# Kernel optimization log

Measured on AMD Instinct MI355X. Metric: run time of the kernel, lower is better.

## Reference

```python
import jax, jax.numpy as jnp
import numpy as np

EMBED_DIM = 1024
NUM_HEADS = 16
HEAD_DIM = EMBED_DIM // NUM_HEADS


def setup_inputs() -> dict:
    key = jax.random.key(0)
    ks = jax.random.split(key, 5)
    B, N, C = 2, 2048, EMBED_DIM
    s = 0.02
    return {
        "x": jax.random.normal(ks[0], (B, N, C), dtype=jnp.float32),
        "w_qkv": jax.random.normal(ks[1], (C, 3 * C), dtype=jnp.float32) * s,
        "b_qkv": jax.random.normal(ks[2], (3 * C,), dtype=jnp.float32) * s,
        "w_proj": jax.random.normal(ks[3], (C, C), dtype=jnp.float32) * s,
        "b_proj": jax.random.normal(ks[4], (C,), dtype=jnp.float32) * s,
    }


def reference(x, w_qkv, b_qkv, w_proj, b_proj):
    B, N, C = x.shape
    H, D = NUM_HEADS, C // NUM_HEADS
    scale = D ** -0.5
    qkv = x @ w_qkv + b_qkv                      # [B,N,3C]
    qkv = qkv.reshape(B, N, 3, H, D).transpose(2, 0, 3, 1, 4)  # [3,B,H,N,D]
    q, k, v = qkv[0] * scale, qkv[1], qkv[2]
    attn = jnp.einsum("bhnd,bhmd->bhnm", q, k)   # [B,H,N,N]
    attn = jax.nn.softmax(attn, axis=-1)
    out = jnp.einsum("bhnm,bhmd->bhnd", attn, v)  # [B,H,N,D]
    out = out.transpose(0, 2, 1, 3).reshape(B, N, C)
    return out @ w_proj + b_proj
```

## Files before the change

### kernel.cpp

```cpp
#include <hip/hip_runtime.h>

typedef short bf16x8 __attribute__((ext_vector_type(8)));
typedef float f32x4 __attribute__((ext_vector_type(4)));
typedef float f32x16 __attribute__((ext_vector_type(16)));
typedef unsigned short ushort8 __attribute__((ext_vector_type(8)));
typedef unsigned short ushort4v __attribute__((ext_vector_type(4)));
typedef unsigned int uint4v __attribute__((ext_vector_type(4)));
typedef unsigned short u16;

__device__ inline u16 f2bf(float f) {
  unsigned int u = __float_as_uint(f);
  u += 0x7fffu + ((u >> 16) & 1u);
  return (u16)(u >> 16);
}

__device__ inline unsigned cvt_pk_bf16(float lo, float hi2) {
  unsigned r;
  asm("v_cvt_pk_bf16_f32 %0, %1, %2" : "=v"(r) : "v"(lo), "v"(hi2));
  return r;
}

__device__ inline void perm32swap(unsigned& a, unsigned& b) {
  asm("v_permlane32_swap_b32 %0, %1" : "+v"(a), "+v"(b));
}

__device__ inline void gload_lds16(const u16* g, u16* l) {
  __builtin_amdgcn_global_load_lds(
      (const __attribute__((address_space(1))) unsigned int*)g,
      (__attribute__((address_space(3))) unsigned int*)l, 16, 0, 0);
}

__global__ __launch_bounds__(256) void cvt_bf16(const float* __restrict__ in,
                                                u16* __restrict__ out, int n) {
  int i = (blockIdx.x * 256 + threadIdx.x) * 8;
  if (i >= n) return;
  float4 a = *(const float4*)(in + i);
  float4 b = *(const float4*)(in + i + 4);
  ushort8 o;
  o[0] = f2bf(a.x); o[1] = f2bf(a.y); o[2] = f2bf(a.z); o[3] = f2bf(a.w);
  o[4] = f2bf(b.x); o[5] = f2bf(b.y); o[6] = f2bf(b.z); o[7] = f2bf(b.w);
  *(ushort8*)(out + i) = o;
}

__global__ __launch_bounds__(256) void trans_w(const float* __restrict__ W,
                                               u16* __restrict__ Wt, int K, int N) {
  const int k0 = blockIdx.x * 64, n0 = blockIdx.y * 64;
  const int tx = threadIdx.x & 63, ty = threadIdx.x >> 6;
  __shared__ float t[64][65];
#pragma unroll
  for (int i = 0; i < 16; ++i) {
    int r = i * 4 + ty;
    t[r][tx] = W[(size_t)(k0 + r) * N + n0 + tx];
  }
  __syncthreads();
#pragma unroll
  for (int i = 0; i < 16; ++i) {
    int r = i * 4 + ty;
    Wt[(size_t)(n0 + r) * K + k0 + tx] = f2bf(t[tx][r]);
  }
}

template <int MODE>
__global__ __launch_bounds__(256) void gemm_bt(
    const u16* __restrict__ A, const u16* __restrict__ Bt, int M, int N, int K,
    const float* __restrict__ bias, float* __restrict__ outF,
    u16* __restrict__ Qb, u16* __restrict__ Kb, u16* __restrict__ Vb) {
  const int bm = blockIdx.x * 128;
  const int bn = blockIdx.y * 128;
  const int tid = threadIdx.x;
  const int wid = tid >> 6;
  const int lr = tid & 15;
  const int lg = (tid >> 4) & 3;
  const int wr = wid >> 1, wc = wid & 1;

  __shared__ u16 smem[32768];
  u16* Ab0 = smem;
  u16* Ab1 = smem + 8192;
  u16* Bb0 = smem + 16384;
  u16* Bb1 = smem + 24576;

  f32x4 acc[4][4] = {};

  const int rowi = tid >> 3;
  const int sslot = ((tid & 7) ^ (rowi & 7)) * 8;
  const u16* Ag = A + (size_t)bm * K;
  const u16* Bg = Bt + (size_t)bn * K;
  const int nkt = K >> 6;

  auto stage = [&](u16* Ad, u16* Bd, int kt) {
    const int kof = kt << 6;
#pragma unroll
    for (int i = 0; i < 4; ++i) {
      const int row = i * 32 + rowi;
      gload_lds16(Ag + (size_t)row * K + kof + sslot, Ad + (i * 32 + wid * 8) * 64);
      gload_lds16(Bg + (size_t)row * K + kof + sslot, Bd + (i * 32 + wid * 8) * 64);
    }
  };

  stage(Ab0, Bb0, 0);
  __syncthreads();

  for (int kt = 0; kt < nkt; ++kt) {
    const int p = kt & 1;
    const char* Ard = (const char*)(p ? Ab1 : Ab0);
    const char* Brd = (const char*)(p ? Bb1 : Bb0);
    bf16x8 af[4], bfr[4];
#pragma unroll
    for (int t = 0; t < 4; ++t) {
      const int ra = wr * 64 + t * 16 + lr;
      const int rb = wc * 64 + t * 16 + lr;
      af[t] = *(const bf16x8*)(Ard + ra * 128 + ((lg * 16) ^ ((ra & 7) << 4)));
      bfr[t] = *(const bf16x8*)(Brd + rb * 128 + ((lg * 16) ^ ((rb & 7) << 4)));
    }
    if (kt + 1 < nkt) stage(p ? Ab0 : Ab1, p ? Bb0 : Bb1, kt + 1);
    __builtin_amdgcn_s_setprio(1);
#pragma unroll
    for (int mt = 0; mt < 4; ++mt)
#pragma unroll
      for (int nt = 0; nt < 4; ++nt)
        acc[mt][nt] = __builtin_amdgcn_mfma_f32_16x16x32_bf16(
            af[mt], bfr[nt], acc[mt][nt], 0, 0, 0);
    __builtin_amdgcn_s_setprio(0);
#pragma unroll
    for (int t = 0; t < 4; ++t) {
      const int ra = wr * 64 + t * 16 + lr;
      const int rb = wc * 64 + t * 16 + lr;
      af[t] = *(const bf16x8*)(Ard + ra * 128 + ((64 + lg * 16) ^ ((ra & 7) << 4)));
      bfr[t] = *(const bf16x8*)(Brd + rb * 128 + ((64 + lg * 16) ^ ((rb & 7) << 4)));
    }
    __builtin_amdgcn_s_setprio(1);
#pragma unroll
    for (int mt = 0; mt < 4; ++mt)
#pragma unroll
      for (int nt = 0; nt < 4; ++nt)
        acc[mt][nt] = __builtin_amdgcn_mfma_f32_16x16x32_bf16(
            af[mt], bfr[nt], acc[mt][nt], 0, 0, 0);
    __builtin_amdgcn_s_setprio(0);
    __syncthreads();
  }

  if (MODE == 1) {
#pragma unroll
    for (int mt = 0; mt < 4; ++mt) {
      const int row0 = bm + wr * 64 + mt * 16 + lg * 4;
#pragma unroll
      for (int nt = 0; nt < 4; ++nt) {
        const int col = bn + wc * 64 + nt * 16 + lr;
        const float bv = bias[col];
#pragma unroll
        for (int r = 0; r < 4; ++r)
          outF[(size_t)(row0 + r) * N + col] = acc[mt][nt][r] + bv;
      }
    }
    return;
  }

  u16* T = smem;
  const int which = bn >> 10;

  if (which == 2) {
#pragma unroll
    for (int nt = 0; nt < 4; ++nt) {
      const int cl = wc * 64 + nt * 16 + lr;
      const float bv = bias[bn + cl];
#pragma unroll
      for (int mt = 0; mt < 4; ++mt) {
        const int rlb = wr * 128 + mt * 32 + lg * 8;
        ushort4v pk;
#pragma unroll
        for (int r = 0; r < 4; ++r) pk[r] = f2bf(acc[mt][nt][r] + bv);
        *(ushort4v*)((char*)T + cl * 256 + (rlb ^ ((cl & 7) << 4))) = pk;
      }
    }
  } else {
    const float sc = (which == 0) ? 0.18033688f : 1.0f;
#pragma unroll
    for (int mt = 0; mt < 4; ++mt) {
      const int rl0 = wr * 64 + mt * 16 + lg * 4;
#pragma unroll
      for (int nt = 0; nt < 4; ++nt) {
        const int cl = wc * 64 + nt * 16 + lr;
        const float bv = bias[bn + cl];
#pragma unroll
        for (int r = 0; r < 4; ++r) {
          const int rl = rl0 + r;
          *(u16*)((char*)T + rl * 256 + ((cl * 2) ^ ((rl & 7) << 4))) =
              f2bf((acc[mt][nt][r] + bv) * sc);
        }
      }
    }
  }
  __syncthreads();

  const int b = bm >> 11;
  const int nbase = bm & 2047;
  if (which == 0) {
#pragma unroll
    for (int i = 0; i < 8; ++i) {
      const int c = i * 256 + tid;
      const int rl = c >> 4, dch = c & 15;
      uint4v v =
          *(const uint4v*)((const char*)T + rl * 256 + ((dch * 16) ^ ((rl & 7) << 4)));
      const int bh = b * 16 + (bn >> 6) + (dch >> 3);
      *(uint4v*)(Qb + ((size_t)bh * 2048 + nbase + rl) * 64 + (dch & 7) * 8) = v;
    }
  } else if (which == 1) {
#pragma unroll
    for (int i = 0; i < 8; ++i) {
      const int c = i * 256 + tid;
      const int lane = c & 63, s = (c >> 6) & 7, ktl = (c >> 9) & 1, hl = c >> 10;
      const int lq = lane & 31, hi2 = lane >> 5;
      const int rl = ktl * 64 + (s & 1) * 32 + lq;
      const int cc = hl * 128 + (s >> 1) * 32 + hi2 * 16;
      uint4v v = *(const uint4v*)((const char*)T + rl * 256 + (cc ^ ((rl & 7) << 4)));
      const int bh = b * 16 + ((bn & 1023) >> 6) + hl;
      const int kt2 = (nbase >> 6) + ktl;
      *(uint4v*)(Kb + ((((size_t)bh * 32 + kt2) * 8 + s) * 64 + lane) * 8) = v;
    }
  } else {
#pragma unroll
    for (int i = 0; i < 8; ++i) {
      const int c = i * 256 + tid;
      const int lane = c & 63, s = (c >> 6) & 7, ktl = (c >> 9) & 1, hl = c >> 10;
      const int lq = lane & 31, hi2 = lane >> 5;
      const int cl = hl * 64 + (s & 1) * 32 + lq;
      const int cc = ktl * 128 + (s >> 1) * 32 + hi2 * 16;
      uint4v v = *(const uint4v*)((const char*)T + cl * 256 + (cc ^ ((cl & 7) << 4)));
      const int bh = b * 16 + ((bn & 1023) >> 6) + hl;
      const int kt2 = (nbase >> 6) + ktl;
      *(uint4v*)(Vb + ((((size_t)bh * 32 + kt2) * 8 + s) * 64 + lane) * 8) = v;
    }
  }
}

__global__ __launch_bounds__(256, 2) void flash_attn10(const u16* __restrict__ Qb,
                                                       const u16* __restrict__ Kp,
                                                       const u16* __restrict__ Vp,
                                                       u16* __restrict__ AO) {
  const int bh = blockIdx.x & 31;
  const int qt = blockIdx.x >> 5;
  const int tid = threadIdx.x;
  const int w = tid >> 6;
  const int lane = tid & 63;
  const int lq = lane & 31;
  const int hi = lane >> 5;
  const int q0 = qt * 128 + w * 32;

  __shared__ u16 Kld[2][4096];
  __shared__ u16 Vld[2][4096];

  const u16* Qg = Qb + ((size_t)bh * 2048 + q0 + lq) * 64 + 8 * hi;
  bf16x8 qf[4];
#pragma unroll
  for (int t = 0; t < 4; ++t) qf[t] = *(const bf16x8*)(Qg + 16 * t);

  const u16* Kg = Kp + (size_t)bh * (32 * 4096);
  const u16* Vg = Vp + (size_t)bh * (32 * 4096);

  f32x16 ot0 = {}, ot1 = {};
  float lacc[8] = {};

  auto stage = [&](int p, int kt) {
    const size_t src = (size_t)kt * 4096;
    gload_lds16(Kg + src + tid * 8, &Kld[p][tid * 8]);
    gload_lds16(Kg + src + 2048 + tid * 8, &Kld[p][2048 + tid * 8]);
    gload_lds16(Vg + src + tid * 8, &Vld[p][tid * 8]);
    gload_lds16(Vg + src + 2048 + tid * 8, &Vld[p][2048 + tid * 8]);
  };

  stage(0, 0);
  __syncthreads();

  for (int kt = 0; kt < 32; ++kt) {
    const int p = kt & 1;
    if (kt < 31) stage(p ^ 1, kt + 1);

    bf16x8 kf[8];
#pragma unroll
    for (int s = 0; s < 8; ++s)
      kf[s] = *(const bf16x8*)&Kld[p][s * 512 + lane * 8];

    f32x16 sa = {}, sb = {};
    __builtin_amdgcn_s_setprio(1);
#pragma unroll
    for (int t = 0; t < 4; ++t) {
      sa = __builtin_amdgcn_mfma_f32_32x32x16_bf16(kf[2 * t], qf[t], sa, 0, 0, 0);
      sb = __builtin_amdgcn_mfma_f32_32x32x16_bf16(kf[2 * t + 1], qf[t], sb, 0, 0, 0);
    }
    __builtin_amdgcn_s_setprio(0);

    bf16x8 vf[8];
#pragma unroll
    for (int s = 0; s < 8; ++s)
      vf[s] = *(const bf16x8*)&Vld[p][s * 512 + lane * 8];

#pragma unroll
    for (int r = 0; r < 16; ++r) {
      sa[r] = __builtin_amdgcn_exp2f(sa[r]);
      sb[r] = __builtin_amdgcn_exp2f(sb[r]);
    }
#pragma unroll
    for (int r = 0; r < 8; ++r)
      lacc[r] += (sa[r] + sa[r + 8]) + (sb[r] + sb[r + 8]);

    unsigned Ua[8], Ub[8];
#pragma unroll
    for (int s = 0; s < 4; ++s)
#pragma unroll
      for (int m2 = 0; m2 < 2; ++m2) {
        Ua[s * 2 + m2] = cvt_pk_bf16(sa[4 * s + 2 * m2], sa[4 * s + 2 * m2 + 1]);
        Ub[s * 2 + m2] = cvt_pk_bf16(sb[4 * s + 2 * m2], sb[4 * s + 2 * m2 + 1]);
      }
    bf16x8 pfrag[4];
#pragma unroll
    for (int t = 0; t < 4; ++t) {
      const unsigned* U = (t < 2) ? Ua : Ub;
      const int tt = t & 1;
      unsigned w0 = U[(2 * tt) * 2 + 0], w2 = U[(2 * tt + 1) * 2 + 0];
      unsigned w1 = U[(2 * tt) * 2 + 1], w3 = U[(2 * tt + 1) * 2 + 1];
      perm32swap(w0, w2);
      perm32swap(w1, w3);
      uint4v uu = {w0, w1, w2, w3};
      pfrag[t] = __builtin_bit_cast(bf16x8, uu);
    }

    __builtin_amdgcn_s_setprio(1);
#pragma unroll
    for (int t = 0; t < 4; ++t) {
      ot0 = __builtin_amdgcn_mfma_f32_32x32x16_bf16(vf[2 * t], pfrag[t], ot0, 0, 0, 0);
      ot1 = __builtin_amdgcn_mfma_f32_32x32x16_bf16(vf[2 * t + 1], pfrag[t], ot1, 0, 0, 0);
    }
    __builtin_amdgcn_s_setprio(0);

    __syncthreads();
  }

  float lsum = ((lacc[0] + lacc[1]) + (lacc[2] + lacc[3])) +
               ((lacc[4] + lacc[5]) + (lacc[6] + lacc[7]));
  lsum += __shfl_xor(lsum, 32, 64);
  const float inv = 1.0f / lsum;

  const int b = bh >> 4, h = bh & 15;
  u16* Ao = AO + ((size_t)(b * 2048 + q0 + lq)) * 1024 + h * 64;
#pragma unroll
  for (int s = 0; s < 4; ++s) {
    {
      const int d = 8 * s + 4 * hi;
      ushort4v pk;
#pragma unroll
      for (int i = 0; i < 4; ++i) pk[i] = f2bf(ot0[4 * s + i] * inv);
      *(ushort4v*)(Ao + d) = pk;
    }
    {
      const int d = 32 + 8 * s + 4 * hi;
      ushort4v pk;
#pragma unroll
      for (int i = 0; i < 4; ++i) pk[i] = f2bf(ot1[4 * s + i] * inv);
      *(ushort4v*)(Ao + d) = pk;
    }
  }
}

extern "C" void kernel_launch(void* const* d_in, const int* in_sizes, int n_in,
                              void* d_out, int out_size, void* d_ws, size_t ws_size,
                              hipStream_t stream) {
  const float* x = (const float*)d_in[0];
  const float* w_qkv = (const float*)d_in[1];
  const float* b_qkv = (const float*)d_in[2];
  const float* w_proj = (const float*)d_in[3];
  const float* b_proj = (const float*)d_in[4];
  float* out = (float*)d_out;

  char* ws = (char*)d_ws;
  u16* xb = (u16*)(ws);
  u16* wqT = (u16*)(ws + (8ull << 20));
  u16* wpT = (u16*)(ws + (14ull << 20));
  u16* Qb = (u16*)(ws + (16ull << 20));
  u16* Kp = (u16*)(ws + (24ull << 20));
  u16* Vp = (u16*)(ws + (32ull << 20));
  u16* AO = (u16*)(ws + (40ull << 20));

  cvt_bf16<<<dim3(2048), dim3(256), 0, stream>>>(x, xb, 4194304);
  trans_w<<<dim3(16, 48), dim3(256), 0, stream>>>(w_qkv, wqT, 1024, 3072);
  trans_w<<<dim3(16, 16), dim3(256), 0, stream>>>(w_proj, wpT, 1024, 1024);
  gemm_bt<0><<<dim3(32, 24), dim3(256), 0, stream>>>(xb, wqT, 4096, 3072, 1024,
                                                     b_qkv, nullptr, Qb, Kp, Vp);
  flash_attn10<<<dim3(512), dim3(256), 0, stream>>>(Qb, Kp, Vp, AO);
  gemm_bt<1><<<dim3(32, 8), dim3(256), 0, stream>>>(AO, wpT, 4096, 1024, 1024,
                                                    b_proj, out, nullptr, nullptr,
                                                    nullptr);
}
```

Before: 108.5 us.

## Deepen flash attention K/V pipeline to four LDS stages with explicit vmcnt waits

Replaces the double-buffered K/V staging in the attention kernel with a four-slot ring that keeps three tiles in flight, using explicit s_waitcnt vmcnt counts and a single barrier per iteration instead of a full __syncthreads after compute. The aim is to hide global-to-LDS load latency more deeply and drop one barrier per tile. LDS per block doubles to 64KB, which may limit residency to two blocks per CU, and the hand-tuned vmcnt values depend on each thread issuing exactly four loads per stage.

```diff
diff --git a/kernel.cpp b/kernel.cpp
--- a/kernel.cpp
+++ b/kernel.cpp
@@ -29,6 +29,12 @@
       (const __attribute__((address_space(1))) unsigned int*)g,
       (__attribute__((address_space(3))) unsigned int*)l, 16, 0, 0);
 }
+
+#define WAITVM(NSTR)                          \
+  do {                                        \
+    asm volatile("s_waitcnt vmcnt(" NSTR ")"); \
+    __builtin_amdgcn_sched_barrier(0);        \
+  } while (0)
 
 __global__ __launch_bounds__(256) void cvt_bf16(const float* __restrict__ in,
                                                 u16* __restrict__ out, int n) {
@@ -233,7 +239,7 @@
   }
 }
 
-__global__ __launch_bounds__(256, 2) void flash_attn10(const u16* __restrict__ Qb,
+__global__ __launch_bounds__(256, 2) void flash_attn11(const u16* __restrict__ Qb,
                                                        const u16* __restrict__ Kp,
                                                        const u16* __restrict__ Vp,
                                                        u16* __restrict__ AO) {
@@ -246,8 +252,8 @@
   const int hi = lane >> 5;
   const int q0 = qt * 128 + w * 32;
 
-  __shared__ u16 Kld[2][4096];
-  __shared__ u16 Vld[2][4096];
+  __shared__ u16 Kld[4][4096];
+  __shared__ u16 Vld[4][4096];
 
   const u16* Qg = Qb + ((size_t)bh * 2048 + q0 + lq) * 64 + 8 * hi;
   bf16x8 qf[4];
@@ -260,25 +266,19 @@
   f32x16 ot0 = {}, ot1 = {};
   float lacc[8] = {};
 
-  auto stage = [&](int p, int kt) {
+  auto stage = [&](int slot, int kt) {
     const size_t src = (size_t)kt * 4096;
-    gload_lds16(Kg + src + tid * 8, &Kld[p][tid * 8]);
-    gload_lds16(Kg + src + 2048 + tid * 8, &Kld[p][2048 + tid * 8]);
-    gload_lds16(Vg + src + tid * 8, &Vld[p][tid * 8]);
-    gload_lds16(Vg + src + 2048 + tid * 8, &Vld[p][2048 + tid * 8]);
+    gload_lds16(Kg + src + tid * 8, &Kld[slot][tid * 8]);
+    gload_lds16(Kg + src + 2048 + tid * 8, &Kld[slot][2048 + tid * 8]);
+    gload_lds16(Vg + src + tid * 8, &Vld[slot][tid * 8]);
+    gload_lds16(Vg + src + 2048 + tid * 8, &Vld[slot][2048 + tid * 8]);
   };
 
-  stage(0, 0);
-  __syncthreads();
-
-  for (int kt = 0; kt < 32; ++kt) {
-    const int p = kt & 1;
-    if (kt < 31) stage(p ^ 1, kt + 1);
-
+  auto compute = [&](int slot) {
     bf16x8 kf[8];
 #pragma unroll
     for (int s = 0; s < 8; ++s)
-      kf[s] = *(const bf16x8*)&Kld[p][s * 512 + lane * 8];
+      kf[s] = *(const bf16x8*)&Kld[slot][s * 512 + lane * 8];
 
     f32x16 sa = {}, sb = {};
     __builtin_amdgcn_s_setprio(1);
@@ -292,7 +292,7 @@
     bf16x8 vf[8];
 #pragma unroll
     for (int s = 0; s < 8; ++s)
-      vf[s] = *(const bf16x8*)&Vld[p][s * 512 + lane * 8];
+      vf[s] = *(const bf16x8*)&Vld[slot][s * 512 + lane * 8];
 
 #pragma unroll
     for (int r = 0; r < 16; ++r) {
@@ -331,9 +331,27 @@
       ot1 = __builtin_amdgcn_mfma_f32_32x32x16_bf16(vf[2 * t + 1], pfrag[t], ot1, 0, 0, 0);
     }
     __builtin_amdgcn_s_setprio(0);
-
-    __syncthreads();
-  }
+  };
+
+  stage(0, 0);
+  stage(1, 1);
+  stage(2, 2);
+
+  for (int kt = 0; kt < 29; ++kt) {
+    WAITVM("8");
+    __builtin_amdgcn_s_barrier();
+    stage((kt + 3) & 3, kt + 3);
+    compute(kt & 3);
+  }
+  WAITVM("8");
+  __builtin_amdgcn_s_barrier();
+  compute(29 & 3);
+  WAITVM("4");
+  __builtin_amdgcn_s_barrier();
+  compute(30 & 3);
+  WAITVM("0");
+  __builtin_amdgcn_s_barrier();
+  compute(31 & 3);
 
   float lsum = ((lacc[0] + lacc[1]) + (lacc[2] + lacc[3])) +
                ((lacc[4] + lacc[5]) + (lacc[6] + lacc[7]));
@@ -385,7 +403,7 @@
   trans_w<<<dim3(16, 16), dim3(256), 0, stream>>>(w_proj, wpT, 1024, 1024);
   gemm_bt<0><<<dim3(32, 24), dim3(256), 0, stream>>>(xb, wqT, 4096, 3072, 1024,
                                                      b_qkv, nullptr, Qb, Kp, Vp);
-  flash_attn10<<<dim3(512), dim3(256), 0, stream>>>(Qb, Kp, Vp, AO);
+  flash_attn11<<<dim3(512), dim3(256), 0, stream>>>(Qb, Kp, Vp, AO);
   gemm_bt<1><<<dim3(32, 8), dim3(256), 0, stream>>>(AO, wpT, 4096, 1024, 1024,
                                                     b_proj, out, nullptr, nullptr,
                                                     nullptr);
```

New measurement: 109.9 us. About the same (+1.3%).

## Split attention KV range across two wave groups; shrink QKV GEMM k-tile for occupancy

Applied to the files above, without the earlier changes.

The flash attention kernel now runs 512 threads per block. Two groups of four waves each process half of the key/value tiles for the same queries, and their partial outputs and row sums are merged through shared memory at the end. This doubles the waves available to hide latency, at the cost of a reduction step and more shared memory per block. The QKV GEMM is split into its own kernel with a 32-wide k-tile and half the LDS, using a new swizzle and launch bounds of 2 blocks per SM to raise occupancy. The projection GEMM keeps the original 64-wide tile.

```diff
diff --git a/kernel.cpp b/kernel.cpp
--- a/kernel.cpp
+++ b/kernel.cpp
@@ -60,11 +60,11 @@
   }
 }
 
-template <int MODE>
-__global__ __launch_bounds__(256) void gemm_bt(
-    const u16* __restrict__ A, const u16* __restrict__ Bt, int M, int N, int K,
-    const float* __restrict__ bias, float* __restrict__ outF,
-    u16* __restrict__ Qb, u16* __restrict__ Kb, u16* __restrict__ Vb) {
+__global__ __launch_bounds__(256, 2) void gemm_qkv(
+    const u16* __restrict__ A, const u16* __restrict__ Bt,
+    const float* __restrict__ bias, u16* __restrict__ Qb,
+    u16* __restrict__ Kb, u16* __restrict__ Vb) {
+  const int K = 1024;
   const int bm = blockIdx.x * 128;
   const int bn = blockIdx.y * 128;
   const int tid = threadIdx.x;
@@ -73,34 +73,31 @@
   const int lg = (tid >> 4) & 3;
   const int wr = wid >> 1, wc = wid & 1;
 
-  __shared__ u16 smem[32768];
+  __shared__ u16 smem[16384];
   u16* Ab0 = smem;
-  u16* Ab1 = smem + 8192;
-  u16* Bb0 = smem + 16384;
-  u16* Bb1 = smem + 24576;
+  u16* Ab1 = smem + 4096;
+  u16* Bb0 = smem + 8192;
+  u16* Bb1 = smem + 12288;
 
   f32x4 acc[4][4] = {};
 
-  const int rowi = tid >> 3;
-  const int sslot = ((tid & 7) ^ (rowi & 7)) * 8;
+  const int srow = tid >> 2;
+  const int scol = ((tid & 3) ^ ((srow >> 1) & 3)) * 8;
   const u16* Ag = A + (size_t)bm * K;
   const u16* Bg = Bt + (size_t)bn * K;
-  const int nkt = K >> 6;
 
   auto stage = [&](u16* Ad, u16* Bd, int kt) {
-    const int kof = kt << 6;
-#pragma unroll
-    for (int i = 0; i < 4; ++i) {
-      const int row = i * 32 + rowi;
-      gload_lds16(Ag + (size_t)row * K + kof + sslot, Ad + (i * 32 + wid * 8) * 64);
-      gload_lds16(Bg + (size_t)row * K + kof + sslot, Bd + (i * 32 + wid * 8) * 64);
-    }
+    const int kof = kt << 5;
+    gload_lds16(Ag + (size_t)srow * K + kof + scol, Ad + tid * 8);
+    gload_lds16(Ag + (size_t)(srow + 64) * K + kof + scol, Ad + 2048 + tid * 8);
+    gload_lds16(Bg + (size_t)srow * K + kof + scol, Bd + tid * 8);
+    gload_lds16(Bg + (size_t)(srow + 64) * K + kof + scol, Bd + 2048 + tid * 8);
   };
 
   stage(Ab0, Bb0, 0);
   __syncthreads();
 
-  for (int kt = 0; kt < nkt; ++kt) {
+  for (int kt = 0; kt < 32; ++kt) {
     const int p = kt & 1;
     const char* Ard = (const char*)(p ? Ab1 : Ab0);
     const char* Brd = (const char*)(p ? Bb1 : Bb0);
@@ -109,25 +106,10 @@
     for (int t = 0; t < 4; ++t) {
       const int ra = wr * 64 + t * 16 + lr;
       const int rb = wc * 64 + t * 16 + lr;
-      af[t] = *(const bf16x8*)(Ard + ra * 128 + ((lg * 16) ^ ((ra & 7) << 4)));
-      bfr[t] = *(const bf16x8*)(Brd + rb * 128 + ((lg * 16) ^ ((rb & 7) << 4)));
-    }
-    if (kt + 1 < nkt) stage(p ? Ab0 : Ab1, p ? Bb0 : Bb1, kt + 1);
-    __builtin_amdgcn_s_setprio(1);
-#pragma unroll
-    for (int mt = 0; mt < 4; ++mt)
-#pragma unroll
-      for (int nt = 0; nt < 4; ++nt)
-        acc[mt][nt] = __builtin_amdgcn_mfma_f32_16x16x32_bf16(
-            af[mt], bfr[nt], acc[mt][nt], 0, 0, 0);
-    __builtin_amdgcn_s_setprio(0);
-#pragma unroll
-    for (int t = 0; t < 4; ++t) {
-      const int ra = wr * 64 + t * 16 + lr;
-      const int rb = wc * 64 + t * 16 + lr;
-      af[t] = *(const bf16x8*)(Ard + ra * 128 + ((64 + lg * 16) ^ ((ra & 7) << 4)));
-      bfr[t] = *(const bf16x8*)(Brd + rb * 128 + ((64 + lg * 16) ^ ((rb & 7) << 4)));
-    }
+      af[t] = *(const bf16x8*)(Ard + ra * 64 + ((lg ^ ((ra >> 1) & 3)) * 16));
+      bfr[t] = *(const bf16x8*)(Brd + rb * 64 + ((lg ^ ((rb >> 1) & 3)) * 16));
+    }
+    if (kt + 1 < 32) stage(p ? Ab0 : Ab1, p ? Bb0 : Bb1, kt + 1);
     __builtin_amdgcn_s_setprio(1);
 #pragma unroll
     for (int mt = 0; mt < 4; ++mt)
@@ -137,22 +119,6 @@
             af[mt], bfr[nt], acc[mt][nt], 0, 0, 0);
     __builtin_amdgcn_s_setprio(0);
     __syncthreads();
-  }
-
-  if (MODE == 1) {
-#pragma unroll
-    for (int mt = 0; mt < 4; ++mt) {
-      const int row0 = bm + wr * 64 + mt * 16 + lg * 4;
-#pragma unroll
-      for (int nt = 0; nt < 4; ++nt) {
-        const int col = bn + wc * 64 + nt * 16 + lr;
-        const float bv = bias[col];
-#pragma unroll
-        for (int r = 0; r < 4; ++r)
-          outF[(size_t)(row0 + r) * N + col] = acc[mt][nt][r] + bv;
-      }
-    }
-    return;
   }
 
   u16* T = smem;
@@ -233,7 +199,98 @@
   }
 }
 
-__global__ __launch_bounds__(256, 2) void flash_attn10(const u16* __restrict__ Qb,
+__global__ __launch_bounds__(256) void gemm_proj(
+    const u16* __restrict__ A, const u16* __restrict__ Bt, int M, int N, int K,
+    const float* __restrict__ bias, float* __restrict__ outF) {
+  const int bm = blockIdx.x * 128;
+  const int bn = blockIdx.y * 128;
+  const int tid = threadIdx.x;
+  const int wid = tid >> 6;
+  const int lr = tid & 15;
+  const int lg = (tid >> 4) & 3;
+  const int wr = wid >> 1, wc = wid & 1;
+
+  __shared__ u16 smem[32768];
+  u16* Ab0 = smem;
+  u16* Ab1 = smem + 8192;
+  u16* Bb0 = smem + 16384;
+  u16* Bb1 = smem + 24576;
+
+  f32x4 acc[4][4] = {};
+
+  const int rowi = tid >> 3;
+  const int sslot = ((tid & 7) ^ (rowi & 7)) * 8;
+  const u16* Ag = A + (size_t)bm * K;
+  const u16* Bg = Bt + (size_t)bn * K;
+  const int nkt = K >> 6;
+
+  auto stage = [&](u16* Ad, u16* Bd, int kt) {
+    const int kof = kt << 6;
+#pragma unroll
+    for (int i = 0; i < 4; ++i) {
+      const int row = i * 32 + rowi;
+      gload_lds16(Ag + (size_t)row * K + kof + sslot, Ad + (i * 32 + wid * 8) * 64);
+      gload_lds16(Bg + (size_t)row * K + kof + sslot, Bd + (i * 32 + wid * 8) * 64);
+    }
+  };
+
+  stage(Ab0, Bb0, 0);
+  __syncthreads();
+
+  for (int kt = 0; kt < nkt; ++kt) {
+    const int p = kt & 1;
+    const char* Ard = (const char*)(p ? Ab1 : Ab0);
+    const char* Brd = (const char*)(p ? Bb1 : Bb0);
+    bf16x8 af[4], bfr[4];
+#pragma unroll
+    for (int t = 0; t < 4; ++t) {
+      const int ra = wr * 64 + t * 16 + lr;
+      const int rb = wc * 64 + t * 16 + lr;
+      af[t] = *(const bf16x8*)(Ard + ra * 128 + ((lg * 16) ^ ((ra & 7) << 4)));
+      bfr[t] = *(const bf16x8*)(Brd + rb * 128 + ((lg * 16) ^ ((rb & 7) << 4)));
+    }
+    if (kt + 1 < nkt) stage(p ? Ab0 : Ab1, p ? Bb0 : Bb1, kt + 1);
+    __builtin_amdgcn_s_setprio(1);
+#pragma unroll
+    for (int mt = 0; mt < 4; ++mt)
+#pragma unroll
+      for (int nt = 0; nt < 4; ++nt)
+        acc[mt][nt] = __builtin_amdgcn_mfma_f32_16x16x32_bf16(
+            af[mt], bfr[nt], acc[mt][nt], 0, 0, 0);
+    __builtin_amdgcn_s_setprio(0);
+#pragma unroll
+    for (int t = 0; t < 4; ++t) {
+      const int ra = wr * 64 + t * 16 + lr;
+      const int rb = wc * 64 + t * 16 + lr;
+      af[t] = *(const bf16x8*)(Ard + ra * 128 + ((64 + lg * 16) ^ ((ra & 7) << 4)));
+      bfr[t] = *(const bf16x8*)(Brd + rb * 128 + ((64 + lg * 16) ^ ((rb & 7) << 4)));
+    }
+    __builtin_amdgcn_s_setprio(1);
+#pragma unroll
+    for (int mt = 0; mt < 4; ++mt)
+#pragma unroll
+      for (int nt = 0; nt < 4; ++nt)
+        acc[mt][nt] = __builtin_amdgcn_mfma_f32_16x16x32_bf16(
+            af[mt], bfr[nt], acc[mt][nt], 0, 0, 0);
+    __builtin_amdgcn_s_setprio(0);
+    __syncthreads();
+  }
+
+#pragma unroll
+  for (int mt = 0; mt < 4; ++mt) {
+    const int row0 = bm + wr * 64 + mt * 16 + lg * 4;
+#pragma unroll
+    for (int nt = 0; nt < 4; ++nt) {
+      const int col = bn + wc * 64 + nt * 16 + lr;
+      const float bv = bias[col];
+#pragma unroll
+      for (int r = 0; r < 4; ++r)
+        outF[(size_t)(row0 + r) * N + col] = acc[mt][nt][r] + bv;
+    }
+  }
+}
+
+__global__ __launch_bounds__(512, 2) void flash_attn13(const u16* __restrict__ Qb,
                                                        const u16* __restrict__ Kp,
                                                        const u16* __restrict__ Vp,
                                                        u16* __restrict__ AO) {
@@ -241,13 +298,14 @@
   const int qt = blockIdx.x >> 5;
   const int tid = threadIdx.x;
   const int w = tid >> 6;
+  const int qw = w & 3;
+  const int half = w >> 2;
   const int lane = tid & 63;
   const int lq = lane & 31;
   const int hi = lane >> 5;
-  const int q0 = qt * 128 + w * 32;
-
-  __shared__ u16 Kld[2][4096];
-  __shared__ u16 Vld[2][4096];
+  const int q0 = qt * 128 + qw * 32;
+
+  __shared__ u16 smem[32768];
 
   const u16* Qg = Qb + ((size_t)bh * 2048 + q0 + lq) * 64 + 8 * hi;
   bf16x8 qf[4];
@@ -260,25 +318,23 @@
   f32x16 ot0 = {}, ot1 = {};
   float lacc[8] = {};
 
-  auto stage = [&](int p, int kt) {
-    const size_t src = (size_t)kt * 4096;
-    gload_lds16(Kg + src + tid * 8, &Kld[p][tid * 8]);
-    gload_lds16(Kg + src + 2048 + tid * 8, &Kld[p][2048 + tid * 8]);
-    gload_lds16(Vg + src + tid * 8, &Vld[p][tid * 8]);
-    gload_lds16(Vg + src + 2048 + tid * 8, &Vld[p][2048 + tid * 8]);
+  auto stage = [&](int buf, int ph) {
+#pragma unroll
+    for (int h = 0; h < 2; ++h) {
+      const size_t src = (size_t)(h * 16 + ph) * 4096;
+      gload_lds16(Kg + src + tid * 8, smem + (buf * 2 + h) * 4096 + tid * 8);
+      gload_lds16(Vg + src + tid * 8, smem + 16384 + (buf * 2 + h) * 4096 + tid * 8);
+    }
   };
 
-  stage(0, 0);
-  __syncthreads();
-
-  for (int kt = 0; kt < 32; ++kt) {
-    const int p = kt & 1;
-    if (kt < 31) stage(p ^ 1, kt + 1);
+  auto compute = [&](int buf) {
+    const u16* Kl = smem + (buf * 2 + half) * 4096;
+    const u16* Vl = smem + 16384 + (buf * 2 + half) * 4096;
 
     bf16x8 kf[8];
 #pragma unroll
     for (int s = 0; s < 8; ++s)
-      kf[s] = *(const bf16x8*)&Kld[p][s * 512 + lane * 8];
+      kf[s] = *(const bf16x8*)&Kl[s * 512 + lane * 8];
 
     f32x16 sa = {}, sb = {};
     __builtin_amdgcn_s_setprio(1);
@@ -292,7 +348,7 @@
     bf16x8 vf[8];
 #pragma unroll
     for (int s = 0; s < 8; ++s)
-      vf[s] = *(const bf16x8*)&Vld[p][s * 512 + lane * 8];
+      vf[s] = *(const bf16x8*)&Vl[s * 512 + lane * 8];
 
 #pragma unroll
     for (int r = 0; r < 16; ++r) {
@@ -331,14 +387,38 @@
       ot1 = __builtin_amdgcn_mfma_f32_32x32x16_bf16(vf[2 * t + 1], pfrag[t], ot1, 0, 0, 0);
     }
     __builtin_amdgcn_s_setprio(0);
-
+  };
+
+  stage(0, 0);
+  __syncthreads();
+
+  for (int ph = 0; ph < 16; ++ph) {
+    const int p = ph & 1;
+    if (ph < 15) stage(p ^ 1, ph + 1);
+    compute(p);
     __syncthreads();
   }
 
   float lsum = ((lacc[0] + lacc[1]) + (lacc[2] + lacc[3])) +
                ((lacc[4] + lacc[5]) + (lacc[6] + lacc[7]));
   lsum += __shfl_xor(lsum, 32, 64);
-  const float inv = 1.0f / lsum;
+
+  float* mp = (float*)smem + ((size_t)qw * 64 + lane) * 33;
+  if (half == 1) {
+#pragma unroll
+    for (int r = 0; r < 16; ++r) mp[r] = ot0[r];
+#pragma unroll
+    for (int r = 0; r < 16; ++r) mp[16 + r] = ot1[r];
+    mp[32] = lsum;
+  }
+  __syncthreads();
+  if (half == 1) return;
+
+  const float inv = 1.0f / (lsum + mp[32]);
+#pragma unroll
+  for (int r = 0; r < 16; ++r) ot0[r] = (ot0[r] + mp[r]) * inv;
+#pragma unroll
+  for (int r = 0; r < 16; ++r) ot1[r] = (ot1[r] + mp[16 + r]) * inv;
 
   const int b = bh >> 4, h = bh & 15;
   u16* Ao = AO + ((size_t)(b * 2048 + q0 + lq)) * 1024 + h * 64;
@@ -348,14 +428,14 @@
       const int d = 8 * s + 4 * hi;
       ushort4v pk;
 #pragma unroll
-      for (int i = 0; i < 4; ++i) pk[i] = f2bf(ot0[4 * s + i] * inv);
+      for (int i = 0; i < 4; ++i) pk[i] = f2bf(ot0[4 * s + i]);
       *(ushort4v*)(Ao + d) = pk;
     }
     {
       const int d = 32 + 8 * s + 4 * hi;
       ushort4v pk;
 #pragma unroll
-      for (int i = 0; i < 4; ++i) pk[i] = f2bf(ot1[4 * s + i] * inv);
+      for (int i = 0; i < 4; ++i) pk[i] = f2bf(ot1[4 * s + i]);
       *(ushort4v*)(Ao + d) = pk;
     }
   }
@@ -383,10 +463,8 @@
   cvt_bf16<<<dim3(2048), dim3(256), 0, stream>>>(x, xb, 4194304);
   trans_w<<<dim3(16, 48), dim3(256), 0, stream>>>(w_qkv, wqT, 1024, 3072);
   trans_w<<<dim3(16, 16), dim3(256), 0, stream>>>(w_proj, wpT, 1024, 1024);
-  gemm_bt<0><<<dim3(32, 24), dim3(256), 0, stream>>>(xb, wqT, 4096, 3072, 1024,
-                                                     b_qkv, nullptr, Qb, Kp, Vp);
-  flash_attn10<<<dim3(512), dim3(256), 0, stream>>>(Qb, Kp, Vp, AO);
-  gemm_bt<1><<<dim3(32, 8), dim3(256), 0, stream>>>(AO, wpT, 4096, 1024, 1024,
-                                                    b_proj, out, nullptr, nullptr,
-                                                    nullptr);
-}
+  gemm_qkv<<<dim3(32, 24), dim3(256), 0, stream>>>(xb, wqT, b_qkv, Qb, Kp, Vp);
+  flash_attn13<<<dim3(512), dim3(512), 0, stream>>>(Qb, Kp, Vp, AO);
+  gemm_proj<<<dim3(32, 8), dim3(256), 0, stream>>>(AO, wpT, 4096, 1024, 1024,
+                                                   b_proj, out);
+}
```

After: 106.1 us. -2.2%, faster.
